# Kernel tuning notes

Measured on AMD Instinct MI355X. Metric: run time of the kernel, lower is better.

Reference implementation:

```python
import jax, jax.numpy as jnp
import numpy as np

B, T, C = 4, 4096, 1024
NH, DH = 16, 128          # n_head, d_head = d_qkv // n_head
DQKV, DR = 2048, 256      # d_qkv, d_rank


def _uniform(key, shape, bound):
    return jax.random.uniform(key, shape, jnp.float32, -bound, bound)


def setup_inputs() -> dict:
    key = jax.random.key(0)
    k0, k1, k2, k3, k4 = jax.random.split(key, 5)
    # CastedLinear init: bound = sqrt(3) * 0.5 * in_features**-0.5 (same for w1, w2)
    b_qkv = (3 ** 0.5) * 0.5 * C ** (-0.5)
    b_proj = (3 ** 0.5) * 0.5 * DQKV ** (-0.5)
    return {
        "x": jax.random.normal(k0, (B, T, C), jnp.float32),
        "qkv_w1": _uniform(k1, (DR, C), b_qkv),
        "qkv_w2": _uniform(k2, (3 * DQKV, DR), b_qkv),
        "cproj_w1": _uniform(k3, (DR, DQKV), b_proj),
        "cproj_w2": _uniform(k4, (2 * C, DR), b_proj),
    }


def _rmsnorm(x):
    eps = jnp.finfo(x.dtype).eps  # F.rms_norm default eps
    return x * jax.lax.rsqrt(jnp.mean(x * x, axis=-1, keepdims=True) + eps)


def reference(x, qkv_w1, qkv_w2, cproj_w1, cproj_w2):
    Bx, Tx, Cx = x.shape
    # qkv projection with low-rank factorization + relu^2 activation between factors
    h = _rmsnorm(x) @ qkv_w1.T                      # [B,T,DR]
    h = jnp.square(jax.nn.relu(h))
    qkv = (h @ qkv_w2.T).reshape(Bx, Tx, 3 * NH, DH)
    q, k, v = jnp.split(qkv, 3, axis=2)             # each [B,T,NH,DH]
    q, k = _rmsnorm(q), _rmsnorm(k)

    # rotary embedding: half the head dim rotated, second quarter frequencies zero
    quarter = DH // 4
    freq = (1.0 / 1024.0) ** jnp.linspace(0.0, 1.0, quarter)
    freq = jnp.concatenate([freq, jnp.zeros(quarter, freq.dtype)])  # [DH//2]
    theta = jnp.arange(Tx, dtype=jnp.float32)[:, None] * freq[None, :]
    cos = jnp.cos(theta)[None, :, None, :]          # [1,T,1,DH//2]
    sin = jnp.sin(theta)[None, :, None, :]

    def rope(z):
        z1, z2 = jnp.split(z, 2, axis=-1)
        return jnp.concatenate([z1 * cos + z2 * sin, -z1 * sin + z2 * cos], axis=-1)

    q, k = rope(q), rope(k)

    # causal linear attention: sigmoid-gated cumulative sum over time
    y = jax.nn.relu(q) * jnp.cumsum(jax.nn.sigmoid(k) * v, axis=1)  # [B,T,NH,DH]
    y = y.reshape(Bx, Tx, NH * DH)

    # low-rank output projection (no activation), gated residual
    uv = (y @ cproj_w1.T) @ cproj_w2.T              # [B,T,2C]
    u, g = jnp.split(uv, 2, axis=-1)
    return x + u * jax.nn.silu(g)
```

## Files before the change

### kernel.cpp

```cpp
#include <hip/hip_runtime.h>
#include <hip/hip_bf16.h>

#define TB 4
#define TT 4096
#define TC 1024
#define TNH 16
#define TDH 128
#define TDQKV 2048
#define TDR 256
#define RB 4096
#define ROWS (TB*TT)
#define SLAB (RB*128)
#define NSEG 128
#define SEGT 32

typedef __attribute__((ext_vector_type(8))) short bfx8;
typedef __attribute__((ext_vector_type(4))) float fx4;
typedef __attribute__((address_space(1))) const unsigned char GAS;
typedef __attribute__((address_space(3))) unsigned char LAS;

__device__ __forceinline__ unsigned short f2b(float f) {
    unsigned int u = __float_as_uint(f);
    unsigned int r = (u + 0x7fffu + ((u >> 16) & 1u)) >> 16;
    return (unsigned short)r;
}
__device__ __forceinline__ float b2f(unsigned short h) {
    return __uint_as_float(((unsigned int)h) << 16);
}
__device__ __forceinline__ float sigm(float x) {
    return 1.0f / (1.0f + __expf(-x));
}
__device__ __forceinline__ int xcd_swz(int hw, int nwg) {
    int q = nwg >> 3;
    return (hw & 7) * q + (hw >> 3);
}

__global__ __launch_bounds__(256) void cvt_bf16(const float* __restrict__ in,
                                                unsigned short* __restrict__ out, int n) {
    int i = (blockIdx.x * 256 + threadIdx.x) * 4;
    if (i < n) {
        float4 v = *(const float4*)(in + i);
        out[i + 0] = f2b(v.x);
        out[i + 1] = f2b(v.y);
        out[i + 2] = f2b(v.z);
        out[i + 3] = f2b(v.w);
    }
}

__global__ __launch_bounds__(256) void rope_tab(float* __restrict__ ct, float* __restrict__ st) {
    int i = blockIdx.x * 256 + threadIdx.x;
    int t = i >> 5, j = i & 31;
    float fr = exp2f(-10.0f * (float)j / 31.0f);
    float th = (float)t * fr;
    ct[i] = cosf(th);
    st[i] = sinf(th);
}

__global__ __launch_bounds__(256) void rmsnorm_x(const float* __restrict__ x,
                                                 unsigned short* __restrict__ xn) {
    int row = blockIdx.x;
    int tid = threadIdx.x;
    float4 v = *(const float4*)(x + (size_t)row * TC + tid * 4);
    float ss = v.x * v.x + v.y * v.y + v.z * v.z + v.w * v.w;
    #pragma unroll
    for (int o = 32; o > 0; o >>= 1) ss += __shfl_xor(ss, o);
    __shared__ float red[4];
    if ((tid & 63) == 0) red[tid >> 6] = ss;
    __syncthreads();
    float tot = red[0] + red[1] + red[2] + red[3];
    float sc = rsqrtf(tot * (1.0f / TC) + 1.1920929e-7f);
    unsigned short* o = xn + (size_t)row * TC + tid * 4;
    o[0] = f2b(v.x * sc); o[1] = f2b(v.y * sc); o[2] = f2b(v.z * sc); o[3] = f2b(v.w * sc);
}

template <int EPI>
__global__ __launch_bounds__(256) void gemm_bt(const unsigned short* __restrict__ A, int lda,
                                               const unsigned short* __restrict__ Bm,
                                               unsigned short* __restrict__ C, int ldc,
                                               int N, int K) {
    __shared__ unsigned short As[2][128 * 32];
    __shared__ unsigned short Bs[2][128 * 32];
    const int m0 = blockIdx.y * 128;
    const int n0 = blockIdx.x * 128;
    const int tid = threadIdx.x;
    const int lane = tid & 63;
    const int w = tid >> 6;
    const int wr = w >> 1, wc = w & 1;
    const int r16 = lane & 15;
    const int kk = (lane >> 4) * 8;
    const int l4 = lane >> 2;
    const int c8 = (lane & 3) * 8;
    const int nk = K >> 5;
    fx4 acc[4][4] = {};

    auto stage = [&](int buf, int k0) {
        #pragma unroll
        for (int i = 0; i < 2; ++i) {
            int rr = (w + 4 * i) * 16 + l4;
            const unsigned short* ga = A + (size_t)(m0 + rr) * lda + k0 + c8;
            const unsigned short* gb = Bm + (size_t)(n0 + rr) * K + k0 + c8;
            __builtin_amdgcn_global_load_lds((GAS*)ga, (LAS*)&As[buf][(w + 4 * i) * 512], 16, 0, 0);
            __builtin_amdgcn_global_load_lds((GAS*)gb, (LAS*)&Bs[buf][(w + 4 * i) * 512], 16, 0, 0);
        }
    };

    stage(0, 0);
    __syncthreads();
    int buf = 0;
    for (int ks = 0; ks < nk; ++ks) {
        if (ks + 1 < nk) stage(buf ^ 1, (ks + 1) * 32);
        bfx8 af[4], bfr[4];
        #pragma unroll
        for (int mi = 0; mi < 4; mi++) af[mi] = *(const bfx8*)&As[buf][(wr * 64 + mi * 16 + r16) * 32 + kk];
        #pragma unroll
        for (int ni = 0; ni < 4; ni++) bfr[ni] = *(const bfx8*)&Bs[buf][(wc * 64 + ni * 16 + r16) * 32 + kk];
        #pragma unroll
        for (int mi = 0; mi < 4; mi++)
            #pragma unroll
            for (int ni = 0; ni < 4; ni++)
                acc[mi][ni] = __builtin_amdgcn_mfma_f32_16x16x32_bf16(af[mi], bfr[ni], acc[mi][ni], 0, 0, 0);
        __syncthreads();
        buf ^= 1;
    }

    const int rg = lane >> 4;
    #pragma unroll
    for (int mi = 0; mi < 4; mi++)
        #pragma unroll
        for (int ni = 0; ni < 4; ni++) {
            int col = n0 + wc * 64 + ni * 16 + r16;
            #pragma unroll
            for (int r = 0; r < 4; r++) {
                int row = m0 + wr * 64 + mi * 16 + rg * 4 + r;
                float v = acc[mi][ni][r];
                if (EPI == 1) { v = fmaxf(v, 0.0f); v *= v; }
                if (EPI == 2) {
                    int head = col >> 7;
                    C[(size_t)head * SLAB + (size_t)row * 128 + (col & 127)] = f2b(v);
                } else {
                    C[(size_t)row * ldc + col] = f2b(v);
                }
            }
        }
}

template <int EPI, int NX>
__global__ __launch_bounds__(256) void gemm_bt64(const unsigned short* __restrict__ A, int lda,
                                                 const unsigned short* __restrict__ Bm,
                                                 unsigned short* __restrict__ C, int ldc,
                                                 int K) {
    __shared__ unsigned short As[2][64 * 32];
    __shared__ unsigned short Bs[2][64 * 32];
    const int hw = blockIdx.y * gridDim.x + blockIdx.x;
    const int lg = xcd_swz(hw, gridDim.x * gridDim.y);
    const int n0 = (lg % NX) * 64;
    const int m0 = (lg / NX) * 64;
    const int tid = threadIdx.x;
    const int lane = tid & 63;
    const int w = tid >> 6;
    const int wr = w >> 1, wc = w & 1;
    const int r16 = lane & 15;
    const int kk = (lane >> 4) * 8;
    const int l4 = lane >> 2;
    const int c8 = (lane & 3) * 8;
    const int nk = K >> 5;
    fx4 acc[2][2] = {};

    auto stage = [&](int buf, int k0) {
        int rr = w * 16 + l4;
        const unsigned short* ga = A + (size_t)(m0 + rr) * lda + k0 + c8;
        const unsigned short* gb = Bm + (size_t)(n0 + rr) * K + k0 + c8;
        __builtin_amdgcn_global_load_lds((GAS*)ga, (LAS*)&As[buf][w * 512], 16, 0, 0);
        __builtin_amdgcn_global_load_lds((GAS*)gb, (LAS*)&Bs[buf][w * 512], 16, 0, 0);
    };

    stage(0, 0);
    __syncthreads();
    int buf = 0;
    for (int ks = 0; ks < nk; ++ks) {
        if (ks + 1 < nk) stage(buf ^ 1, (ks + 1) * 32);
        bfx8 af[2], bfr[2];
        #pragma unroll
        for (int mi = 0; mi < 2; mi++) af[mi] = *(const bfx8*)&As[buf][(wr * 32 + mi * 16 + r16) * 32 + kk];
        #pragma unroll
        for (int ni = 0; ni < 2; ni++) bfr[ni] = *(const bfx8*)&Bs[buf][(wc * 32 + ni * 16 + r16) * 32 + kk];
        #pragma unroll
        for (int mi = 0; mi < 2; mi++)
            #pragma unroll
            for (int ni = 0; ni < 2; ni++)
                acc[mi][ni] = __builtin_amdgcn_mfma_f32_16x16x32_bf16(af[mi], bfr[ni], acc[mi][ni], 0, 0, 0);
        __syncthreads();
        buf ^= 1;
    }

    const int rg = lane >> 4;
    #pragma unroll
    for (int mi = 0; mi < 2; mi++)
        #pragma unroll
        for (int ni = 0; ni < 2; ni++) {
            int col = n0 + wc * 32 + ni * 16 + r16;
            #pragma unroll
            for (int r = 0; r < 4; r++) {
                int row = m0 + wr * 32 + mi * 16 + rg * 4 + r;
                float v = acc[mi][ni][r];
                if (EPI == 1) { v = fmaxf(v, 0.0f); v *= v; }
                C[(size_t)row * ldc + col] = f2b(v);
            }
        }
}

__global__ __launch_bounds__(256) void gemm4f64(const unsigned short* __restrict__ A,
                                                const unsigned short* __restrict__ Wm,
                                                const float* __restrict__ x,
                                                float* __restrict__ out) {
    __shared__ unsigned short As[2][64 * 32];
    __shared__ unsigned short Bu[2][64 * 32];
    __shared__ unsigned short Bg[2][64 * 32];
    const int hw = blockIdx.y * gridDim.x + blockIdx.x;
    const int lg = xcd_swz(hw, gridDim.x * gridDim.y);
    const int n0 = (lg & 15) * 64;
    const int m0 = (lg >> 4) * 64;
    const int tid = threadIdx.x;
    const int lane = tid & 63;
    const int w = tid >> 6;
    const int wr = w >> 1, wc = w & 1;
    const int r16 = lane & 15;
    const int kk = (lane >> 4) * 8;
    const int l4 = lane >> 2;
    const int c8 = (lane & 3) * 8;
    fx4 accu[2][2] = {};
    fx4 accg[2][2] = {};

    auto stage = [&](int buf, int k0) {
        int rr = w * 16 + l4;
        const unsigned short* ga = A + (size_t)(m0 + rr) * TDR + k0 + c8;
        const unsigned short* gu = Wm + (size_t)(n0 + rr) * TDR + k0 + c8;
        const unsigned short* gg = Wm + (size_t)(1024 + n0 + rr) * TDR + k0 + c8;
        __builtin_amdgcn_global_load_lds((GAS*)ga, (LAS*)&As[buf][w * 512], 16, 0, 0);
        __builtin_amdgcn_global_load_lds((GAS*)gu, (LAS*)&Bu[buf][w * 512], 16, 0, 0);
        __builtin_amdgcn_global_load_lds((GAS*)gg, (LAS*)&Bg[buf][w * 512], 16, 0, 0);
    };

    stage(0, 0);
    __syncthreads();
    int buf = 0;
    for (int ks = 0; ks < 8; ++ks) {
        if (ks + 1 < 8) stage(buf ^ 1, (ks + 1) * 32);
        bfx8 af[2], bu[2], bg[2];
        #pragma unroll
        for (int mi = 0; mi < 2; mi++) af[mi] = *(const bfx8*)&As[buf][(wr * 32 + mi * 16 + r16) * 32 + kk];
        #pragma unroll
        for (int ni = 0; ni < 2; ni++) {
            bu[ni] = *(const bfx8*)&Bu[buf][(wc * 32 + ni * 16 + r16) * 32 + kk];
            bg[ni] = *(const bfx8*)&Bg[buf][(wc * 32 + ni * 16 + r16) * 32 + kk];
        }
        #pragma unroll
        for (int mi = 0; mi < 2; mi++)
            #pragma unroll
            for (int ni = 0; ni < 2; ni++) {
                accu[mi][ni] = __builtin_amdgcn_mfma_f32_16x16x32_bf16(af[mi], bu[ni], accu[mi][ni], 0, 0, 0);
                accg[mi][ni] = __builtin_amdgcn_mfma_f32_16x16x32_bf16(af[mi], bg[ni], accg[mi][ni], 0, 0, 0);
            }
        __syncthreads();
        buf ^= 1;
    }

    const int rg = lane >> 4;
    #pragma unroll
    for (int mi = 0; mi < 2; mi++)
        #pragma unroll
        for (int ni = 0; ni < 2; ni++) {
            int col = n0 + wc * 32 + ni * 16 + r16;
            #pragma unroll
            for (int r = 0; r < 4; r++) {
                int row = m0 + wr * 32 + mi * 16 + rg * 4 + r;
                float u = accu[mi][ni][r];
                float g = accg[mi][ni][r];
                size_t idx = (size_t)row * TC + col;
                out[idx] = x[idx] + u * (g * sigm(g));
            }
        }
}

__global__ __launch_bounds__(256) void post64(unsigned short* __restrict__ qkv,
                                              const float* __restrict__ ct,
                                              const float* __restrict__ st,
                                              float* __restrict__ part) {
    const int blk = blockIdx.x;
    const int tile = blk & 63, h = blk >> 6;
    const int g = threadIdx.x >> 4, l16 = threadIdx.x & 15;
    const int d0 = l16 * 4;
    unsigned short* qs = qkv + (size_t)h * SLAB;
    unsigned short* ks = qkv + (size_t)(16 + h) * SLAB;
    unsigned short* vs = qkv + (size_t)(32 + h) * SLAB;
    __shared__ float psum[2][16][128];
    float acc0[2][4] = {};
    float acc1[2][4] = {};

    #pragma unroll
    for (int p = 0; p < 4; ++p) {
        const int t = tile * 64 + p * 16 + g;
        const size_t lo = (size_t)t * 128 + d0, hi = lo + 64;
        ushort4 q1 = *(const ushort4*)(qs + lo);
        ushort4 q2 = *(const ushort4*)(qs + hi);
        ushort4 k1 = *(const ushort4*)(ks + lo);
        ushort4 k2 = *(const ushort4*)(ks + hi);
        float qa[8] = {b2f(q1.x), b2f(q1.y), b2f(q1.z), b2f(q1.w),
                       b2f(q2.x), b2f(q2.y), b2f(q2.z), b2f(q2.w)};
        float ka[8] = {b2f(k1.x), b2f(k1.y), b2f(k1.z), b2f(k1.w),
                       b2f(k2.x), b2f(k2.y), b2f(k2.z), b2f(k2.w)};
        float ssq = 0.0f, ssk = 0.0f;
        #pragma unroll
        for (int j = 0; j < 8; ++j) { ssq += qa[j] * qa[j]; ssk += ka[j] * ka[j]; }
        #pragma unroll
        for (int o = 8; o > 0; o >>= 1) {
            ssq += __shfl_xor(ssq, o);
            ssk += __shfl_xor(ssk, o);
        }
        float qsc = rsqrtf(ssq * (1.0f / TDH) + 1.1920929e-7f);
        float ksc = rsqrtf(ssk * (1.0f / TDH) + 1.1920929e-7f);
        float c[4], s[4];
        if (l16 < 8) {
            float4 cv = *(const float4*)(ct + t * 32 + d0);
            float4 sv = *(const float4*)(st + t * 32 + d0);
            c[0] = cv.x; c[1] = cv.y; c[2] = cv.z; c[3] = cv.w;
            s[0] = sv.x; s[1] = sv.y; s[2] = sv.z; s[3] = sv.w;
        } else {
            c[0] = c[1] = c[2] = c[3] = 1.0f;
            s[0] = s[1] = s[2] = s[3] = 0.0f;
        }
        ushort4 v1 = *(const ushort4*)(vs + lo);
        ushort4 v2 = *(const ushort4*)(vs + hi);
        float va[8] = {b2f(v1.x), b2f(v1.y), b2f(v1.z), b2f(v1.w),
                       b2f(v2.x), b2f(v2.y), b2f(v2.z), b2f(v2.w)};
        ushort4 qo1, qo2, po1, po2;
        unsigned short* qo1p = (unsigned short*)&qo1;
        unsigned short* qo2p = (unsigned short*)&qo2;
        unsigned short* po1p = (unsigned short*)&po1;
        unsigned short* po2p = (unsigned short*)&po2;
        const int h2 = p >> 1;
        #pragma unroll
        for (int j = 0; j < 4; ++j) {
            float z1q = qa[j] * qsc, z2q = qa[4 + j] * qsc;
            float z1k = ka[j] * ksc, z2k = ka[4 + j] * ksc;
            float qlo = z1q * c[j] + z2q * s[j];
            float qhi = z2q * c[j] - z1q * s[j];
            float klo = z1k * c[j] + z2k * s[j];
            float khi = z2k * c[j] - z1k * s[j];
            float plo = sigm(klo) * va[j];
            float phi = sigm(khi) * va[4 + j];
            qo1p[j] = f2b(qlo); qo2p[j] = f2b(qhi);
            po1p[j] = f2b(plo); po2p[j] = f2b(phi);
            acc0[h2][j] += plo;
            acc1[h2][j] += phi;
        }
        *(ushort4*)(qs + lo) = qo1;
        *(ushort4*)(qs + hi) = qo2;
        *(ushort4*)(ks + lo) = po1;
        *(ushort4*)(ks + hi) = po2;
    }
    #pragma unroll
    for (int h2 = 0; h2 < 2; ++h2) {
        *(float4*)&psum[h2][g][d0]      = *(float4*)acc0[h2];
        *(float4*)&psum[h2][g][64 + d0] = *(float4*)acc1[h2];
    }
    __syncthreads();
    const int h2 = threadIdx.x >> 7, d = threadIdx.x & 127;
    float tot = 0.0f;
    #pragma unroll
    for (int gg = 0; gg < 16; ++gg) tot += psum[h2][gg][d];
    part[((size_t)h * NSEG + tile * 2 + h2) * 128 + d] = tot;
}

__global__ __launch_bounds__(256) void scanB128(float* __restrict__ part) {
    int idx = blockIdx.x * 256 + threadIdx.x;
    int h = idx >> 7, d = idx & 127;
    float run = 0.0f;
    #pragma unroll 8
    for (int s = 0; s < NSEG; ++s) {
        float* p = part + ((size_t)(h * NSEG + s)) * 128 + d;
        float tv = *p;
        *p = run;
        run += tv;
    }
}

__global__ __launch_bounds__(256) void scanC3(const unsigned short* __restrict__ qkv,
                                              const float* __restrict__ part,
                                              unsigned short* __restrict__ y) {
    const int bseg = blockIdx.x & 7, h = blockIdx.x >> 3;
    const int g = threadIdx.x >> 4, l16 = threadIdx.x & 15;
    const int seg = bseg * 16 + g;
    const int d0 = l16 * 8;
    const unsigned short* qp = qkv + (size_t)h * SLAB;
    const unsigned short* pp = qkv + (size_t)(16 + h) * SLAB;
    float sum[8];
    const float* pb = part + ((size_t)(h * NSEG + seg)) * 128 + d0;
    *(float4*)&sum[0] = *(const float4*)pb;
    *(float4*)&sum[4] = *(const float4*)(pb + 4);
    #pragma unroll 4
    for (int i = 0; i < SEGT; ++i) {
        int t = seg * SEGT + i;
        size_t off = (size_t)t * 128 + d0;
        bfx8 pv = *(const bfx8*)(pp + off);
        bfx8 qv = *(const bfx8*)(qp + off);
        bfx8 ov;
        #pragma unroll
        for (int j = 0; j < 8; ++j) {
            sum[j] += b2f((unsigned short)pv[j]);
            float q = b2f((unsigned short)qv[j]);
            ov[j] = (short)f2b(fmaxf(q, 0.0f) * sum[j]);
        }
        *(bfx8*)(y + (size_t)t * 2048 + h * 128 + d0) = ov;
    }
}

extern "C" void kernel_launch(void* const* d_in, const int* in_sizes, int n_in,
                              void* d_out, int out_size, void* d_ws, size_t ws_size,
                              hipStream_t stream) {
    (void)in_sizes; (void)n_in; (void)out_size; (void)ws_size;
    const float* x    = (const float*)d_in[0];
    const float* wq1  = (const float*)d_in[1];
    const float* wq2  = (const float*)d_in[2];
    const float* wc1  = (const float*)d_in[3];
    const float* wc2  = (const float*)d_in[4];
    float* out = (float*)d_out;

    char* ws = (char*)d_ws;
    size_t off = 0;
    auto alloc = [&](size_t bytes) -> void* {
        off = (off + 255) & ~(size_t)255;
        void* p = ws + off;
        off += bytes;
        return p;
    };
    char* pool = (char*)alloc((size_t)RB * 6144 * 2);
    unsigned short* qkvb = (unsigned short*)pool;
    unsigned short* xn   = (unsigned short*)pool;
    unsigned short* t1   = (unsigned short*)pool;
    unsigned short* hbuf = (unsigned short*)alloc((size_t)ROWS * TDR * 2);
    unsigned short* w1b  = (unsigned short*)alloc((size_t)TDR * TC * 2);
    unsigned short* w2b  = (unsigned short*)alloc((size_t)3 * TDQKV * TDR * 2);
    unsigned short* wp1b = (unsigned short*)alloc((size_t)TDR * TDQKV * 2);
    unsigned short* wp2b = (unsigned short*)alloc((size_t)2 * TC * TDR * 2);
    float* ct   = (float*)alloc((size_t)TT * 32 * 4);
    float* st   = (float*)alloc((size_t)TT * 32 * 4);
    float* part = (float*)alloc((size_t)TNH * NSEG * 128 * 4);
    unsigned short* ybuf = (unsigned short*)d_out;

    cvt_bf16<<<(TDR * TC) / 1024, 256, 0, stream>>>(wq1, w1b, TDR * TC);
    cvt_bf16<<<(3 * TDQKV * TDR) / 1024, 256, 0, stream>>>(wq2, w2b, 3 * TDQKV * TDR);
    cvt_bf16<<<(TDR * TDQKV) / 1024, 256, 0, stream>>>(wc1, wp1b, TDR * TDQKV);
    cvt_bf16<<<(2 * TC * TDR) / 1024, 256, 0, stream>>>(wc2, wp2b, 2 * TC * TDR);
    rope_tab<<<(TT * 32) / 256, 256, 0, stream>>>(ct, st);

    rmsnorm_x<<<ROWS, 256, 0, stream>>>(x, xn);
    gemm_bt64<1, 4><<<dim3(TDR / 64, ROWS / 64), 256, 0, stream>>>(
        xn, TC, w1b, hbuf, TDR, TC);

    for (int b = 0; b < TB; ++b) {
        gemm_bt<2><<<dim3(6144 / 128, RB / 128), 256, 0, stream>>>(
            hbuf + (size_t)b * RB * TDR, TDR, w2b, qkvb, 0, 6144, TDR);
        post64<<<TNH * 64, 256, 0, stream>>>(qkvb, ct, st, part);
        scanB128<<<(TNH * 128) / 256, 256, 0, stream>>>(part);
        scanC3<<<TNH * 8, 256, 0, stream>>>(qkvb, part, ybuf + (size_t)b * RB * 2048);
    }

    gemm_bt64<0, 4><<<dim3(TDR / 64, ROWS / 64), 256, 0, stream>>>(
        ybuf, 2048, wp1b, t1, TDR, TDQKV);
    gemm4f64<<<dim3(TC / 64, ROWS / 64), 256, 0, stream>>>(t1, wp2b, x, out);
}
```

Baseline: 383.1 us.

## Merge setup kernels, enlarge skinny GEMM M-tile, prefetch residual in output GEMM

```diff
diff --git a/kernel.cpp b/kernel.cpp
--- a/kernel.cpp
+++ b/kernel.cpp
@@ -35,25 +35,32 @@
     return (hw & 7) * q + (hw >> 3);
 }
 
-__global__ __launch_bounds__(256) void cvt_bf16(const float* __restrict__ in,
-                                                unsigned short* __restrict__ out, int n) {
-    int i = (blockIdx.x * 256 + threadIdx.x) * 4;
-    if (i < n) {
+__global__ __launch_bounds__(256) void setup_all(const float* __restrict__ wq1, unsigned short* __restrict__ w1b,
+                                                 const float* __restrict__ wq2, unsigned short* __restrict__ w2b,
+                                                 const float* __restrict__ wc1, unsigned short* __restrict__ wp1b,
+                                                 const float* __restrict__ wc2, unsigned short* __restrict__ wp2b,
+                                                 float* __restrict__ ct, float* __restrict__ st) {
+    int blk = blockIdx.x;
+    if (blk < 2816) {
+        const float* in; unsigned short* out; int base;
+        if (blk < 256)       { in = wq1; out = w1b;  base = blk; }
+        else if (blk < 1792) { in = wq2; out = w2b;  base = blk - 256; }
+        else if (blk < 2304) { in = wc1; out = wp1b; base = blk - 1792; }
+        else                 { in = wc2; out = wp2b; base = blk - 2304; }
+        int i = (base * 256 + threadIdx.x) * 4;
         float4 v = *(const float4*)(in + i);
         out[i + 0] = f2b(v.x);
         out[i + 1] = f2b(v.y);
         out[i + 2] = f2b(v.z);
         out[i + 3] = f2b(v.w);
-    }
-}
-
-__global__ __launch_bounds__(256) void rope_tab(float* __restrict__ ct, float* __restrict__ st) {
-    int i = blockIdx.x * 256 + threadIdx.x;
-    int t = i >> 5, j = i & 31;
-    float fr = exp2f(-10.0f * (float)j / 31.0f);
-    float th = (float)t * fr;
-    ct[i] = cosf(th);
-    st[i] = sinf(th);
+    } else {
+        int i = (blk - 2816) * 256 + threadIdx.x;
+        int t = i >> 5, j = i & 31;
+        float fr = exp2f(-10.0f * (float)j / 31.0f);
+        float th = (float)t * fr;
+        ct[i] = cosf(th);
+        st[i] = sinf(th);
+    }
 }
 
 __global__ __launch_bounds__(256) void rmsnorm_x(const float* __restrict__ x,
@@ -145,16 +152,15 @@
 }
 
 template <int EPI, int NX>
-__global__ __launch_bounds__(256) void gemm_bt64(const unsigned short* __restrict__ A, int lda,
-                                                 const unsigned short* __restrict__ Bm,
-                                                 unsigned short* __restrict__ C, int ldc,
-                                                 int K) {
-    __shared__ unsigned short As[2][64 * 32];
+__global__ __launch_bounds__(256) void gemm_sk(const unsigned short* __restrict__ A, int lda,
+                                               const unsigned short* __restrict__ Bm,
+                                               unsigned short* __restrict__ C, int ldc,
+                                               int K) {
+    __shared__ unsigned short As[2][128 * 32];
     __shared__ unsigned short Bs[2][64 * 32];
-    const int hw = blockIdx.y * gridDim.x + blockIdx.x;
-    const int lg = xcd_swz(hw, gridDim.x * gridDim.y);
+    const int lg = xcd_swz(blockIdx.x, gridDim.x);
     const int n0 = (lg % NX) * 64;
-    const int m0 = (lg / NX) * 64;
+    const int m0 = (lg / NX) * 128;
     const int tid = threadIdx.x;
     const int lane = tid & 63;
     const int w = tid >> 6;
@@ -164,13 +170,16 @@
     const int l4 = lane >> 2;
     const int c8 = (lane & 3) * 8;
     const int nk = K >> 5;
-    fx4 acc[2][2] = {};
+    fx4 acc[4][2] = {};
 
     auto stage = [&](int buf, int k0) {
-        int rr = w * 16 + l4;
-        const unsigned short* ga = A + (size_t)(m0 + rr) * lda + k0 + c8;
-        const unsigned short* gb = Bm + (size_t)(n0 + rr) * K + k0 + c8;
-        __builtin_amdgcn_global_load_lds((GAS*)ga, (LAS*)&As[buf][w * 512], 16, 0, 0);
+        #pragma unroll
+        for (int i = 0; i < 2; ++i) {
+            int rr = (w + 4 * i) * 16 + l4;
+            const unsigned short* ga = A + (size_t)(m0 + rr) * lda + k0 + c8;
+            __builtin_amdgcn_global_load_lds((GAS*)ga, (LAS*)&As[buf][(w + 4 * i) * 512], 16, 0, 0);
+        }
+        const unsigned short* gb = Bm + (size_t)(n0 + w * 16 + l4) * K + k0 + c8;
         __builtin_amdgcn_global_load_lds((GAS*)gb, (LAS*)&Bs[buf][w * 512], 16, 0, 0);
     };
 
@@ -179,13 +188,13 @@
     int buf = 0;
     for (int ks = 0; ks < nk; ++ks) {
         if (ks + 1 < nk) stage(buf ^ 1, (ks + 1) * 32);
-        bfx8 af[2], bfr[2];
-        #pragma unroll
-        for (int mi = 0; mi < 2; mi++) af[mi] = *(const bfx8*)&As[buf][(wr * 32 + mi * 16 + r16) * 32 + kk];
+        bfx8 af[4], bfr[2];
+        #pragma unroll
+        for (int mi = 0; mi < 4; mi++) af[mi] = *(const bfx8*)&As[buf][(wr * 64 + mi * 16 + r16) * 32 + kk];
         #pragma unroll
         for (int ni = 0; ni < 2; ni++) bfr[ni] = *(const bfx8*)&Bs[buf][(wc * 32 + ni * 16 + r16) * 32 + kk];
         #pragma unroll
-        for (int mi = 0; mi < 2; mi++)
+        for (int mi = 0; mi < 4; mi++)
             #pragma unroll
             for (int ni = 0; ni < 2; ni++)
                 acc[mi][ni] = __builtin_amdgcn_mfma_f32_16x16x32_bf16(af[mi], bfr[ni], acc[mi][ni], 0, 0, 0);
@@ -195,13 +204,13 @@
 
     const int rg = lane >> 4;
     #pragma unroll
-    for (int mi = 0; mi < 2; mi++)
+    for (int mi = 0; mi < 4; mi++)
         #pragma unroll
         for (int ni = 0; ni < 2; ni++) {
             int col = n0 + wc * 32 + ni * 16 + r16;
             #pragma unroll
             for (int r = 0; r < 4; r++) {
-                int row = m0 + wr * 32 + mi * 16 + rg * 4 + r;
+                int row = m0 + wr * 64 + mi * 16 + rg * 4 + r;
                 float v = acc[mi][ni][r];
                 if (EPI == 1) { v = fmaxf(v, 0.0f); v *= v; }
                 C[(size_t)row * ldc + col] = f2b(v);
@@ -225,7 +234,8 @@
     const int w = tid >> 6;
     const int wr = w >> 1, wc = w & 1;
     const int r16 = lane & 15;
-    const int kk = (lane >> 4) * 8;
+    const int rg = lane >> 4;
+    const int kk = rg * 8;
     const int l4 = lane >> 2;
     const int c8 = (lane & 3) * 8;
     fx4 accu[2][2] = {};
@@ -242,6 +252,15 @@
     };
 
     stage(0, 0);
+    float xr[2][2][4];
+    #pragma unroll
+    for (int mi = 0; mi < 2; mi++)
+        #pragma unroll
+        for (int ni = 0; ni < 2; ni++)
+            #pragma unroll
+            for (int r = 0; r < 4; r++)
+                xr[mi][ni][r] = x[(size_t)(m0 + wr * 32 + mi * 16 + rg * 4 + r) * TC
+                                  + n0 + wc * 32 + ni * 16 + r16];
     __syncthreads();
     int buf = 0;
     for (int ks = 0; ks < 8; ++ks) {
@@ -265,7 +284,6 @@
         buf ^= 1;
     }
 
-    const int rg = lane >> 4;
     #pragma unroll
     for (int mi = 0; mi < 2; mi++)
         #pragma unroll
@@ -276,8 +294,7 @@
                 int row = m0 + wr * 32 + mi * 16 + rg * 4 + r;
                 float u = accu[mi][ni][r];
                 float g = accg[mi][ni][r];
-                size_t idx = (size_t)row * TC + col;
-                out[idx] = x[idx] + u * (g * sigm(g));
+                out[(size_t)row * TC + col] = xr[mi][ni][r] + u * (g * sigm(g));
             }
         }
 }
@@ -448,14 +465,10 @@
     float* part = (float*)alloc((size_t)TNH * NSEG * 128 * 4);
     unsigned short* ybuf = (unsigned short*)d_out;
 
-    cvt_bf16<<<(TDR * TC) / 1024, 256, 0, stream>>>(wq1, w1b, TDR * TC);
-    cvt_bf16<<<(3 * TDQKV * TDR) / 1024, 256, 0, stream>>>(wq2, w2b, 3 * TDQKV * TDR);
-    cvt_bf16<<<(TDR * TDQKV) / 1024, 256, 0, stream>>>(wc1, wp1b, TDR * TDQKV);
-    cvt_bf16<<<(2 * TC * TDR) / 1024, 256, 0, stream>>>(wc2, wp2b, 2 * TC * TDR);
-    rope_tab<<<(TT * 32) / 256, 256, 0, stream>>>(ct, st);
+    setup_all<<<3328, 256, 0, stream>>>(wq1, w1b, wq2, w2b, wc1, wp1b, wc2, wp2b, ct, st);
 
     rmsnorm_x<<<ROWS, 256, 0, stream>>>(x, xn);
-    gemm_bt64<1, 4><<<dim3(TDR / 64, ROWS / 64), 256, 0, stream>>>(
+    gemm_sk<1, 4><<<(ROWS / 128) * (TDR / 64), 256, 0, stream>>>(
         xn, TC, w1b, hbuf, TDR, TC);
 
     for (int b = 0; b < TB; ++b) {
@@ -466,7 +479,7 @@
         scanC3<<<TNH * 8, 256, 0, stream>>>(qkvb, part, ybuf + (size_t)b * RB * 2048);
     }
 
-    gemm_bt64<0, 4><<<dim3(TDR / 64, ROWS / 64), 256, 0, stream>>>(
+    gemm_sk<0, 4><<<(ROWS / 128) * (TDR / 64), 256, 0, stream>>>(
         ybuf, 2048, wp1b, t1, TDR, TDQKV);
     gemm4f64<<<dim3(TC / 64, ROWS / 64), 256, 0, stream>>>(t1, wp2b, x, out);
 }
```

New measurement: 376.9 us. About the same (-1.6%).
